# Optimization experiments

Measured on AMD Instinct MI355X. Metric: run time of the kernel, lower is better.

The kernel has to match this reference:

```python
import jax, jax.numpy as jnp
import numpy as np

MARGIN = 0.1
EPS = 1e-8  # torch CosineSimilarity eps


def setup_inputs() -> dict:
    key = jax.random.key(0)
    k1, k2 = jax.random.split(key)
    embeddings = jax.random.normal(k1, (8192, 128), dtype=jnp.float32)
    labels = jax.random.randint(k2, (8192,), 0, 100, dtype=jnp.int64 if jax.config.jax_enable_x64 else jnp.int32)
    return {"embeddings": embeddings, "labels": labels}


def reference(embeddings, labels):
    n = embeddings.shape[0]
    # Normalize rows (torch: x / max(||x||, eps))
    norm = jnp.linalg.norm(embeddings, axis=1, keepdims=True)
    en = embeddings / jnp.maximum(norm, EPS)
    # Full cosine-similarity matrix via one GEMM: [n, n]
    sim = jnp.einsum('id,jd->ij', en, en)
    same = labels[:, None] == labels[None, :]
    pair_loss = jnp.where(same, jax.nn.relu(1.0 - sim), jax.nn.relu(sim - MARGIN))
    # Sum over i < j (strict upper triangle), matching the double loop
    upper = jnp.triu(jnp.ones((n, n), dtype=pair_loss.dtype), k=1)
    loss = jnp.sum(pair_loss * upper) / (n * (n - 1))
    return loss
```

## Files before the change

### kernel.cpp

```cpp
#include <hip/hip_runtime.h>
#include <hip/hip_bf16.h>


typedef __attribute__((ext_vector_type(8))) short short8;
typedef __attribute__((ext_vector_type(4))) float f32x4;

#define DIM 128
#define MARGIN 0.1f
#define CHUNK 4

typedef const void __attribute__((address_space(1)))* gas_ptr;
typedef void __attribute__((address_space(3)))* las_ptr;

static __device__ __forceinline__ void load16_to_lds(const void* g, void* l) {
    __builtin_amdgcn_global_load_lds((gas_ptr)g, (las_ptr)l, 16, 0, 0);
}

static __device__ __forceinline__ unsigned short f2bf(float f) {
    unsigned int u = __builtin_bit_cast(unsigned int, f);
    u += 0x7FFFu + ((u >> 16) & 1u);
    return (unsigned short)(u >> 16);
}

static __device__ __forceinline__ void stage64(const short* __restrict__ en, int row0,
                                               short* buf, int tid) {
    const char* src = (const char*)(en + (size_t)row0 * DIM);
    char* dst = (char*)buf;
    const int r_lo = tid >> 4;
    const int s    = tid & 15;
    #pragma unroll
    for (int p = 0; p < 4; ++p) {
        const int r  = p * 16 + r_lo;
        const int sc = (s ^ (r & 7)) << 4;
        load16_to_lds(src + (size_t)r * 256 + sc, dst + r * 256 + s * 16);
    }
}

static __device__ __forceinline__ short8 read_frag(const short* buf, int row, int slot) {
    const int ps = slot ^ (row & 7);
    return *(const short8*)(buf + row * DIM + ps * 8);
}

__global__ void __launch_bounds__(256) norm_bf16_kernel(const float* __restrict__ e,
                                                        unsigned int* __restrict__ en_packed) {
    const int row  = blockIdx.x * 4 + (threadIdx.x >> 6);
    const int lane = threadIdx.x & 63;
    const float2 v = *reinterpret_cast<const float2*>(e + row * DIM + lane * 2);
    float s = v.x * v.x + v.y * v.y;
    #pragma unroll
    for (int off = 32; off; off >>= 1) s += __shfl_xor(s, off, 64);
    const float scale = 1.0f / fmaxf(sqrtf(s), 1e-8f);
    const unsigned int lo = f2bf(v.x * scale);
    const unsigned int hi = f2bf(v.y * scale);
    en_packed[row * (DIM / 2) + lane] = (hi << 16) | lo;
}

__global__ void __launch_bounds__(256, 3)
tri_loss_kernel(const short* __restrict__ en, const int* __restrict__ labels,
                float* __restrict__ partials, int nt) {
    __shared__ __align__(16) short buf[2][64 * DIM];
    __shared__ float wsum[4];

    int t  = blockIdx.x;
    int bi = 0, cnt = (nt + CHUNK - 1) / CHUNK;
    #pragma unroll 1
    while (t >= cnt) { t -= cnt; ++bi; cnt = (nt - bi + CHUNK - 1) / CHUNK; }
    const int jbase = bi + t * CHUNK;
    const int nsub  = 2 * min(CHUNK, nt - jbase);

    const int tid  = threadIdx.x;
    const int lane = tid & 63;
    const int wid  = tid >> 6;
    const int wr   = wid >> 1, wc = wid & 1;
    const int lm   = lane & 15;
    const int hi   = lane >> 4;

    stage64(en, bi * 128,      &buf[0][0], tid);
    stage64(en, bi * 128 + 64, &buf[1][0], tid);

    const int r0w = bi * 128 + wr * 64;
    int4 li[4];
    #pragma unroll
    for (int m = 0; m < 4; ++m) li[m] = *(const int4*)(labels + r0w + m * 16 + hi * 4);

    __syncthreads();

    short8 a[4][4];
    const short* Abuf = &buf[wr][0];
    #pragma unroll
    for (int m = 0; m < 4; ++m)
        #pragma unroll
        for (int ks = 0; ks < 4; ++ks)
            a[m][ks] = read_frag(Abuf, m * 16 + lm, hi + ks * 4);

    __syncthreads();

    stage64(en, jbase * 128, &buf[0][0], tid);
    __syncthreads();

    float lsum = 0.0f;
    const int rb = hi * 4;

    #pragma unroll 1
    for (int s = 0; s < nsub; ++s) {
        const short* cur = &buf[s & 1][0];
        if (s + 1 < nsub)
            stage64(en, jbase * 128 + (s + 1) * 64, &buf[(s + 1) & 1][0], tid);

        const int c0 = jbase * 128 + s * 64 + wc * 32;
        int labj[2];
        labj[0] = labels[c0 + lm];
        labj[1] = labels[c0 + 16 + lm];

        f32x4 acc[4][2] = {};
        #pragma unroll
        for (int ks = 0; ks < 4; ++ks) {
            short8 b[2];
            b[0] = read_frag(cur, wc * 32 + lm,      hi + ks * 4);
            b[1] = read_frag(cur, wc * 32 + 16 + lm, hi + ks * 4);
            #pragma unroll
            for (int m = 0; m < 4; ++m)
                #pragma unroll
                for (int n = 0; n < 2; ++n)
                    acc[m][n] = __builtin_amdgcn_mfma_f32_16x16x32_bf16(a[m][ks], b[n], acc[m][n], 0, 0, 0);
        }

        const bool diag = (jbase == bi) && (s < 2);
        #pragma unroll
        for (int m = 0; m < 4; ++m) {
            #pragma unroll
            for (int r = 0; r < 4; ++r) {
                const int i   = r0w + m * 16 + rb + r;
                const int l_i = ((const int*)&li[m])[r];
                #pragma unroll
                for (int n = 0; n < 2; ++n) {
                    const int j  = c0 + n * 16 + lm;
                    const float sv = acc[m][n][r];
                    const float t2 = (l_i == labj[n]) ? (1.0f - sv) : (sv - MARGIN);
                    const float v  = fmaxf(t2, 0.0f);
                    if (!diag || i < j) lsum += v;
                }
            }
        }
        __syncthreads();
    }

    #pragma unroll
    for (int off = 32; off; off >>= 1) lsum += __shfl_down(lsum, off, 64);
    if (lane == 0) wsum[wid] = lsum;
    __syncthreads();
    if (tid == 0) partials[blockIdx.x] = wsum[0] + wsum[1] + wsum[2] + wsum[3];
}

__global__ void __launch_bounds__(256) final_reduce_kernel(const float* __restrict__ partials,
                                                           float* __restrict__ out,
                                                           int n, float inv_denom) {
    float s = 0.0f;
    for (int i = threadIdx.x; i < n; i += 256) s += partials[i];
    #pragma unroll
    for (int off = 32; off; off >>= 1) s += __shfl_xor(s, off, 64);
    __shared__ float wsum[4];
    if ((threadIdx.x & 63) == 0) wsum[threadIdx.x >> 6] = s;
    __syncthreads();
    if (threadIdx.x == 0) out[0] = (wsum[0] + wsum[1] + wsum[2] + wsum[3]) * inv_denom;
}

extern "C" void kernel_launch(void* const* d_in, const int* in_sizes, int n_in,
                              void* d_out, int out_size, void* d_ws, size_t ws_size,
                              hipStream_t stream) {
    const float* emb    = (const float*)d_in[0];
    const int*   labels = (const int*)d_in[1];
    float*       out    = (float*)d_out;

    const int n  = in_sizes[1];
    const int nt = n / 128;

    int Tc = 0;
    for (int i = 0; i < nt; ++i) Tc += (nt - i + CHUNK - 1) / CHUNK;

    unsigned int* en_packed = (unsigned int*)d_ws;
    short*        en        = (short*)d_ws;
    float*        partials  = (float*)((char*)d_ws + (size_t)n * DIM * 2);

    norm_bf16_kernel<<<n / 4, 256, 0, stream>>>(emb, en_packed);

    tri_loss_kernel<<<Tc, 256, 0, stream>>>(en, labels, partials, nt);

    const float inv_denom = (float)(1.0 / ((double)n * (double)(n - 1)));
    final_reduce_kernel<<<1, 256, 0, stream>>>(partials, out, Tc, inv_denom);
}
```

Before: 31.00 us.

## Software-pipeline MFMA of next sub-tile with epilogue of current sub-tile

The sub-tile loop now uses two accumulator sets and two label sets, unrolled by two. The MFMAs for sub-tile s+1 are issued before the loss epilogue of sub-tile s, so matrix and vector work can overlap. LDS staging is also pushed one step further ahead, with B-fragment offsets precomputed once. The epilogue is simplified: the diagonal mask is applied only to diagonal tiles, partial sums accumulate in a float4, and the relu on the same-label term is dropped. Holding twice the accumulators raises register pressure, so launch bounds drop from 3 to 2 blocks per CU.

```diff
diff --git a/kernel.cpp b/kernel.cpp
--- a/kernel.cpp
+++ b/kernel.cpp
@@ -55,7 +55,61 @@
     en_packed[row * (DIM / 2) + lane] = (hi << 16) | lo;
 }
 
-__global__ void __launch_bounds__(256, 3)
+
+#define EPI_FAST(ACC, LJ)                                                          \
+    _Pragma("unroll") for (int m = 0; m < 4; ++m)                                  \
+        _Pragma("unroll") for (int n = 0; n < 2; ++n) {                            \
+            const f32x4 sv   = ACC[m][n];                                          \
+            const f32x4 base = sv - MARGIN;                                        \
+            const f32x4 alt  = 1.0f - sv;                                          \
+            _Pragma("unroll") for (int r = 0; r < 4; ++r) {                        \
+                const float bv = fmaxf(base[r], 0.0f);                             \
+                vsum[r] += (liv[m][r] == LJ[n]) ? alt[r] : bv;                     \
+            }                                                                      \
+        }
+
+#define EPI_DIAG(ACC, LJ)                                                          \
+    _Pragma("unroll") for (int m = 0; m < 4; ++m)                                  \
+        _Pragma("unroll") for (int n = 0; n < 2; ++n) {                            \
+            const f32x4 sv   = ACC[m][n];                                          \
+            const f32x4 base = sv - MARGIN;                                        \
+            const f32x4 alt  = 1.0f - sv;                                          \
+            const int jj = c0 + n * 16 + lm;                                       \
+            _Pragma("unroll") for (int r = 0; r < 4; ++r) {                        \
+                const int ii = r0w + m * 16 + rb + r;                              \
+                const float bv = fmaxf(base[r], 0.0f);                             \
+                const float tv = (liv[m][r] == LJ[n]) ? alt[r] : bv;               \
+                vsum[r] += (ii < jj) ? tv : 0.0f;                                  \
+            }                                                                      \
+        }
+
+#define ITER(SX, BSEL, ACC_C, ACC_N, LJ_C, LJ_N) do {                              \
+    const int sx_ = (SX);                                                          \
+    __syncthreads();                                                               \
+    if (sx_ + 2 < nsub) stage64(en, jb128 + (sx_ + 2) * 64, &buf[sx_ & 1][0], tid);\
+    if (sx_ + 1 < nsub) {                                                          \
+        const int c0n = jb128 + (sx_ + 1) * 64 + wc * 32;                          \
+        LJ_N[0] = labels[c0n + lm];                                                \
+        LJ_N[1] = labels[c0n + 16 + lm];                                           \
+        _Pragma("unroll") for (int m = 0; m < 4; ++m)                              \
+            _Pragma("unroll") for (int n = 0; n < 2; ++n)                          \
+                ACC_N[m][n] = (f32x4){0.0f, 0.0f, 0.0f, 0.0f};                     \
+        _Pragma("unroll") for (int ks = 0; ks < 4; ++ks) {                         \
+            const short8 b0 = *(const short8*)(bbase + (BSEL) * 16384 + boff[0][ks]); \
+            const short8 b1 = *(const short8*)(bbase + (BSEL) * 16384 + boff[1][ks]); \
+            _Pragma("unroll") for (int m = 0; m < 4; ++m) {                        \
+                ACC_N[m][0] = __builtin_amdgcn_mfma_f32_16x16x32_bf16(a[m][ks], b0, ACC_N[m][0], 0, 0, 0); \
+                ACC_N[m][1] = __builtin_amdgcn_mfma_f32_16x16x32_bf16(a[m][ks], b1, ACC_N[m][1], 0, 0, 0); \
+            }                                                                      \
+        }                                                                          \
+    }                                                                              \
+    {                                                                              \
+        const int c0 = jb128 + sx_ * 64 + wc * 32; (void)c0;                       \
+        if (hasdiag && sx_ < 2) { EPI_DIAG(ACC_C, LJ_C) } else { EPI_FAST(ACC_C, LJ_C) } \
+    }                                                                              \
+} while (0)
+
+__global__ void __launch_bounds__(256, 2)
 tri_loss_kernel(const short* __restrict__ en, const int* __restrict__ labels,
                 float* __restrict__ partials, int nt) {
     __shared__ __align__(16) short buf[2][64 * DIM];
@@ -66,7 +120,9 @@
     #pragma unroll 1
     while (t >= cnt) { t -= cnt; ++bi; cnt = (nt - bi + CHUNK - 1) / CHUNK; }
     const int jbase = bi + t * CHUNK;
+    const int jb128 = jbase * 128;
     const int nsub  = 2 * min(CHUNK, nt - jbase);
+    const bool hasdiag = (jbase == bi);
 
     const int tid  = threadIdx.x;
     const int lane = tid & 63;
@@ -74,14 +130,18 @@
     const int wr   = wid >> 1, wc = wid & 1;
     const int lm   = lane & 15;
     const int hi   = lane >> 4;
+    const int rb   = hi * 4;
 
     stage64(en, bi * 128,      &buf[0][0], tid);
     stage64(en, bi * 128 + 64, &buf[1][0], tid);
 
     const int r0w = bi * 128 + wr * 64;
-    int4 li[4];
-    #pragma unroll
-    for (int m = 0; m < 4; ++m) li[m] = *(const int4*)(labels + r0w + m * 16 + hi * 4);
+    int liv[4][4];
+    #pragma unroll
+    for (int m = 0; m < 4; ++m) {
+        const int4 v = *(const int4*)(labels + r0w + m * 16 + rb);
+        liv[m][0] = v.x; liv[m][1] = v.y; liv[m][2] = v.z; liv[m][3] = v.w;
+    }
 
     __syncthreads();
 
@@ -93,58 +153,54 @@
         for (int ks = 0; ks < 4; ++ks)
             a[m][ks] = read_frag(Abuf, m * 16 + lm, hi + ks * 4);
 
-    __syncthreads();
-
-    stage64(en, jbase * 128, &buf[0][0], tid);
-    __syncthreads();
-
-    float lsum = 0.0f;
-    const int rb = hi * 4;
-
-    #pragma unroll 1
-    for (int s = 0; s < nsub; ++s) {
-        const short* cur = &buf[s & 1][0];
-        if (s + 1 < nsub)
-            stage64(en, jbase * 128 + (s + 1) * 64, &buf[(s + 1) & 1][0], tid);
-
-        const int c0 = jbase * 128 + s * 64 + wc * 32;
-        int labj[2];
-        labj[0] = labels[c0 + lm];
-        labj[1] = labels[c0 + 16 + lm];
-
-        f32x4 acc[4][2] = {};
+    const char* bbase = (const char*)&buf[0][0];
+    int boff[2][4];
+    #pragma unroll
+    for (int n = 0; n < 2; ++n) {
+        const int row = wc * 32 + n * 16 + lm;
+        #pragma unroll
+        for (int ks = 0; ks < 4; ++ks)
+            boff[n][ks] = row * 256 + (((hi + ks * 4) ^ (row & 7)) << 4);
+    }
+
+    __syncthreads();
+
+    stage64(en, jb128,      &buf[0][0], tid);
+    stage64(en, jb128 + 64, &buf[1][0], tid);
+    __syncthreads();
+
+    f32x4 accA[4][2], accB[4][2];
+    int   ljA[2], ljB[2];
+    f32x4 vsum = (f32x4){0.0f, 0.0f, 0.0f, 0.0f};
+
+    {
+        const int c00 = jb128 + wc * 32;
+        ljA[0] = labels[c00 + lm];
+        ljA[1] = labels[c00 + 16 + lm];
+        #pragma unroll
+        for (int m = 0; m < 4; ++m)
+            #pragma unroll
+            for (int n = 0; n < 2; ++n)
+                accA[m][n] = (f32x4){0.0f, 0.0f, 0.0f, 0.0f};
         #pragma unroll
         for (int ks = 0; ks < 4; ++ks) {
-            short8 b[2];
-            b[0] = read_frag(cur, wc * 32 + lm,      hi + ks * 4);
-            b[1] = read_frag(cur, wc * 32 + 16 + lm, hi + ks * 4);
+            const short8 b0 = *(const short8*)(bbase + boff[0][ks]);
+            const short8 b1 = *(const short8*)(bbase + boff[1][ks]);
             #pragma unroll
-            for (int m = 0; m < 4; ++m)
-                #pragma unroll
-                for (int n = 0; n < 2; ++n)
-                    acc[m][n] = __builtin_amdgcn_mfma_f32_16x16x32_bf16(a[m][ks], b[n], acc[m][n], 0, 0, 0);
-        }
-
-        const bool diag = (jbase == bi) && (s < 2);
-        #pragma unroll
-        for (int m = 0; m < 4; ++m) {
-            #pragma unroll
-            for (int r = 0; r < 4; ++r) {
-                const int i   = r0w + m * 16 + rb + r;
-                const int l_i = ((const int*)&li[m])[r];
-                #pragma unroll
-                for (int n = 0; n < 2; ++n) {
-                    const int j  = c0 + n * 16 + lm;
-                    const float sv = acc[m][n][r];
-                    const float t2 = (l_i == labj[n]) ? (1.0f - sv) : (sv - MARGIN);
-                    const float v  = fmaxf(t2, 0.0f);
-                    if (!diag || i < j) lsum += v;
-                }
+            for (int m = 0; m < 4; ++m) {
+                accA[m][0] = __builtin_amdgcn_mfma_f32_16x16x32_bf16(a[m][ks], b0, accA[m][0], 0, 0, 0);
+                accA[m][1] = __builtin_amdgcn_mfma_f32_16x16x32_bf16(a[m][ks], b1, accA[m][1], 0, 0, 0);
             }
         }
-        __syncthreads();
-    }
-
+    }
+
+    #pragma unroll 1
+    for (int s = 0; s < nsub; s += 2) {
+        ITER(s,     1, accA, accB, ljA, ljB);
+        ITER(s + 1, 0, accB, accA, ljB, ljA);
+    }
+
+    float lsum = vsum[0] + vsum[1] + vsum[2] + vsum[3];
     #pragma unroll
     for (int off = 32; off; off >>= 1) lsum += __shfl_down(lsum, off, 64);
     if (lane == 0) wsum[wid] = lsum;
```

Measured after the change: 32.90 us. +6.1%, slower.

## Split loss into label-agnostic hinge plus per-class correction pass

Applied to the files above, without the earlier changes.

The main GEMM kernel now applies only relu(sim - margin) to every pair, with no label loads or compares. Same-label pairs are fixed up by a separate pass: labels are bucketed with a histogram and compaction kernels, and a per-class kernel computes those pairs' dot products in fp32 and adds relu(1-s) - relu(s-margin). This removes per-element label comparisons from the hot epilogue. The cost is three extra serial launches, a single-block histogram, a label count hardcoded to 100, and per-class dot products that use bf16-rounded values, so they may differ slightly from the MFMA results they cancel.

```diff
diff --git a/kernel.cpp b/kernel.cpp
--- a/kernel.cpp
+++ b/kernel.cpp
@@ -8,6 +8,9 @@
 #define DIM 128
 #define MARGIN 0.1f
 #define CHUNK 4
+#define NLAB 100
+#define CR 48
+#define PD 132
 
 typedef const void __attribute__((address_space(1)))* gas_ptr;
 typedef void __attribute__((address_space(3)))* las_ptr;
@@ -55,9 +58,120 @@
     en_packed[row * (DIM / 2) + lane] = (hi << 16) | lo;
 }
 
+__global__ void __launch_bounds__(256) count_kernel(const int* __restrict__ labels, int n,
+                                                    int* __restrict__ starts) {
+    __shared__ int hist[NLAB];
+    for (int i = threadIdx.x; i < NLAB; i += 256) hist[i] = 0;
+    __syncthreads();
+    for (int i = threadIdx.x; i < n; i += 256) atomicAdd(&hist[labels[i]], 1);
+    __syncthreads();
+    if (threadIdx.x == 0) {
+        int acc = 0;
+        for (int c = 0; c < NLAB; ++c) { starts[c] = acc; acc += hist[c]; }
+        starts[NLAB] = acc;
+    }
+}
+
+__global__ void __launch_bounds__(256) compact_kernel(const int* __restrict__ labels, int n,
+                                                      const int* __restrict__ starts,
+                                                      int* __restrict__ perm) {
+    const int c    = blockIdx.x;
+    const int tid  = threadIdx.x;
+    const int lane = tid & 63;
+    const int wid  = tid >> 6;
+    __shared__ int wcnt[4];
+    __shared__ int running;
+    if (tid == 0) running = 0;
+    __syncthreads();
+    const int base_c = starts[c];
+    for (int base = 0; base < n; base += 256) {
+        const int i = base + tid;
+        const bool pred = (i < n) && (labels[i] == c);
+        const unsigned long long mask = __ballot(pred);
+        const int myrank = __popcll(mask & ((1ULL << lane) - 1ULL));
+        if (lane == 0) wcnt[wid] = __popcll(mask);
+        __syncthreads();
+        int woff = 0;
+        #pragma unroll
+        for (int w = 0; w < 4; ++w) woff += (w < wid) ? wcnt[w] : 0;
+        const int tot = wcnt[0] + wcnt[1] + wcnt[2] + wcnt[3];
+        if (pred) perm[base_c + running + woff + myrank] = i;
+        __syncthreads();
+        if (tid == 0) running += tot;
+        __syncthreads();
+    }
+}
+
+static __device__ __forceinline__ void stage_rows_f32(const short* __restrict__ en,
+                                                      const int* __restrict__ idx, int nu,
+                                                      float* __restrict__ L, int tid) {
+    for (int q = tid; q < nu * 16; q += 256) {
+        const int k = q >> 4, t = q & 15;
+        const int row = idx[k];
+        const short8 v = *(const short8*)(en + (size_t)row * DIM + t * 8);
+        #pragma unroll
+        for (int e = 0; e < 8; ++e) {
+            const unsigned int u = ((unsigned int)(unsigned short)v[e]) << 16;
+            L[k * PD + t * 8 + e] = __builtin_bit_cast(float, u);
+        }
+    }
+}
+
+__global__ void __launch_bounds__(256) corr_kernel(const short* __restrict__ en,
+                                                   const int* __restrict__ starts,
+                                                   const int* __restrict__ perm,
+                                                   float* __restrict__ outc) {
+    __shared__ float LA[CR * PD];
+    __shared__ float LB[CR * PD];
+    __shared__ float wsum[4];
+    const int c   = blockIdx.x;
+    const int s0  = starts[c];
+    const int nc  = starts[c + 1] - s0;
+    const int tid = threadIdx.x;
+
+    float acc = 0.0f;
+    for (int cu = 0; cu < nc; cu += CR) {
+        const int nu = min(CR, nc - cu);
+        __syncthreads();
+        stage_rows_f32(en, perm + s0 + cu, nu, LA, tid);
+        for (int cv = cu; cv < nc; cv += CR) {
+            const int nv = min(CR, nc - cv);
+            __syncthreads();
+            const float* B = LA;
+            if (cv > cu) { stage_rows_f32(en, perm + s0 + cv, nv, LB, tid); B = LB; }
+            __syncthreads();
+            const bool tri = (cv == cu);
+            const float inv_nv = 1.0f / (float)nv;
+            for (int p = tid; p < nu * nv; p += 256) {
+                int u = (int)((float)p * inv_nv);
+                int v = p - u * nv;
+                if (v < 0)        { --u; v += nv; }
+                else if (v >= nv) { ++u; v -= nv; }
+                if (!tri || u < v) {
+                    const float* pa = &LA[u * PD];
+                    const float* pb = &B[v * PD];
+                    float s = 0.0f;
+                    #pragma unroll
+                    for (int d = 0; d < DIM; d += 4) {
+                        const f32x4 va = *(const f32x4*)(pa + d);
+                        const f32x4 vb = *(const f32x4*)(pb + d);
+                        s += va[0] * vb[0] + va[1] * vb[1] + va[2] * vb[2] + va[3] * vb[3];
+                    }
+                    acc += fmaxf(1.0f - s, 0.0f) - fmaxf(s - MARGIN, 0.0f);
+                }
+            }
+        }
+    }
+
+    #pragma unroll
+    for (int off = 32; off; off >>= 1) acc += __shfl_down(acc, off, 64);
+    if ((tid & 63) == 0) wsum[tid >> 6] = acc;
+    __syncthreads();
+    if (tid == 0) outc[c] = wsum[0] + wsum[1] + wsum[2] + wsum[3];
+}
+
 __global__ void __launch_bounds__(256, 3)
-tri_loss_kernel(const short* __restrict__ en, const int* __restrict__ labels,
-                float* __restrict__ partials, int nt) {
+tri_loss_kernel(const short* __restrict__ en, float* __restrict__ partials, int nt) {
     __shared__ __align__(16) short buf[2][64 * DIM];
     __shared__ float wsum[4];
 
@@ -74,15 +188,12 @@
     const int wr   = wid >> 1, wc = wid & 1;
     const int lm   = lane & 15;
     const int hi   = lane >> 4;
+    const int rb   = hi * 4;
 
     stage64(en, bi * 128,      &buf[0][0], tid);
     stage64(en, bi * 128 + 64, &buf[1][0], tid);
 
     const int r0w = bi * 128 + wr * 64;
-    int4 li[4];
-    #pragma unroll
-    for (int m = 0; m < 4; ++m) li[m] = *(const int4*)(labels + r0w + m * 16 + hi * 4);
-
     __syncthreads();
 
     short8 a[4][4];
@@ -98,19 +209,13 @@
     stage64(en, jbase * 128, &buf[0][0], tid);
     __syncthreads();
 
-    float lsum = 0.0f;
-    const int rb = hi * 4;
+    f32x4 vsum = (f32x4){0.0f, 0.0f, 0.0f, 0.0f};
 
     #pragma unroll 1
     for (int s = 0; s < nsub; ++s) {
         const short* cur = &buf[s & 1][0];
         if (s + 1 < nsub)
             stage64(en, jbase * 128 + (s + 1) * 64, &buf[(s + 1) & 1][0], tid);
-
-        const int c0 = jbase * 128 + s * 64 + wc * 32;
-        int labj[2];
-        labj[0] = labels[c0 + lm];
-        labj[1] = labels[c0 + 16 + lm];
 
         f32x4 acc[4][2] = {};
         #pragma unroll
@@ -125,26 +230,36 @@
                     acc[m][n] = __builtin_amdgcn_mfma_f32_16x16x32_bf16(a[m][ks], b[n], acc[m][n], 0, 0, 0);
         }
 
-        const bool diag = (jbase == bi) && (s < 2);
-        #pragma unroll
-        for (int m = 0; m < 4; ++m) {
+        if ((jbase == bi) && (s < 2)) {
+            const int c0 = jbase * 128 + s * 64 + wc * 32;
             #pragma unroll
-            for (int r = 0; r < 4; ++r) {
-                const int i   = r0w + m * 16 + rb + r;
-                const int l_i = ((const int*)&li[m])[r];
+            for (int m = 0; m < 4; ++m)
                 #pragma unroll
                 for (int n = 0; n < 2; ++n) {
-                    const int j  = c0 + n * 16 + lm;
-                    const float sv = acc[m][n][r];
-                    const float t2 = (l_i == labj[n]) ? (1.0f - sv) : (sv - MARGIN);
-                    const float v  = fmaxf(t2, 0.0f);
-                    if (!diag || i < j) lsum += v;
+                    const f32x4 sv = acc[m][n] - MARGIN;
+                    const int jj = c0 + n * 16 + lm;
+                    #pragma unroll
+                    for (int r = 0; r < 4; ++r) {
+                        const int ii = r0w + m * 16 + rb + r;
+                        const float tv = fmaxf(sv[r], 0.0f);
+                        vsum[r] += (ii < jj) ? tv : 0.0f;
+                    }
                 }
-            }
+        } else {
+            #pragma unroll
+            for (int m = 0; m < 4; ++m)
+                #pragma unroll
+                for (int n = 0; n < 2; ++n) {
+                    const f32x4 sv = acc[m][n] - MARGIN;
+                    #pragma unroll
+                    for (int r = 0; r < 4; ++r)
+                        vsum[r] += fmaxf(sv[r], 0.0f);
+                }
         }
         __syncthreads();
     }
 
+    float lsum = vsum[0] + vsum[1] + vsum[2] + vsum[3];
     #pragma unroll
     for (int off = 32; off; off >>= 1) lsum += __shfl_down(lsum, off, 64);
     if (lane == 0) wsum[wid] = lsum;
@@ -178,14 +293,19 @@
     int Tc = 0;
     for (int i = 0; i < nt; ++i) Tc += (nt - i + CHUNK - 1) / CHUNK;
 
-    unsigned int* en_packed = (unsigned int*)d_ws;
-    short*        en        = (short*)d_ws;
-    float*        partials  = (float*)((char*)d_ws + (size_t)n * DIM * 2);
+    char* ws = (char*)d_ws;
+    unsigned int* en_packed = (unsigned int*)ws;
+    short*        en        = (short*)ws;
+    float*        partials  = (float*)(ws + (size_t)n * DIM * 2);
+    int*          starts    = (int*)(partials + Tc + NLAB);
+    int*          perm      = starts + (NLAB + 1);
 
     norm_bf16_kernel<<<n / 4, 256, 0, stream>>>(emb, en_packed);
-
-    tri_loss_kernel<<<Tc, 256, 0, stream>>>(en, labels, partials, nt);
+    count_kernel<<<1, 256, 0, stream>>>(labels, n, starts);
+    compact_kernel<<<NLAB, 256, 0, stream>>>(labels, n, starts, perm);
+    corr_kernel<<<NLAB, 256, 0, stream>>>(en, starts, perm, partials + Tc);
+    tri_loss_kernel<<<Tc, 256, 0, stream>>>(en, partials, nt);
 
     const float inv_denom = (float)(1.0 / ((double)n * (double)(n - 1)));
-    final_reduce_kernel<<<1, 256, 0, stream>>>(partials, out, Tc, inv_denom);
-}
+    final_reduce_kernel<<<1, 256, 0, stream>>>(partials, out, Tc + NLAB, inv_denom);
+}
```

After: 76.56 us. 2.47x slower.

## Sort rows by label so off-diagonal tiles skip label comparisons

Applied to the files above, without the earlier changes.

Adds a prep kernel that, besides normalising rows to bf16, counting-sorts row indices by label into a permutation and a permuted label array. The loss kernel gathers rows through this permutation, so most tile pairs hold disjoint label ranges and take a cheap hinge-only path with no per-element label compare. The double loop over i<j is symmetric, so permuting rows does not change the result. It hardcodes 100 labels and a per-wave bucket capacity of 160, and adds indirect row loads during staging.

```diff
diff --git a/kernel.cpp b/kernel.cpp
--- a/kernel.cpp
+++ b/kernel.cpp
@@ -8,6 +8,8 @@
 #define DIM 128
 #define MARGIN 0.1f
 #define CHUNK 4
+#define NLAB 100
+#define WCAP 160
 
 typedef const void __attribute__((address_space(1)))* gas_ptr;
 typedef void __attribute__((address_space(3)))* las_ptr;
@@ -22,17 +24,19 @@
     return (unsigned short)(u >> 16);
 }
 
-static __device__ __forceinline__ void stage64(const short* __restrict__ en, int row0,
-                                               short* buf, int tid) {
-    const char* src = (const char*)(en + (size_t)row0 * DIM);
+static __device__ __forceinline__ void stage64p(const short* __restrict__ en,
+                                                const int* __restrict__ perm, int row0,
+                                                short* buf, int tid) {
     char* dst = (char*)buf;
     const int r_lo = tid >> 4;
-    const int s    = tid & 15;
+    const int slot = tid & 15;
     #pragma unroll
     for (int p = 0; p < 4; ++p) {
-        const int r  = p * 16 + r_lo;
-        const int sc = (s ^ (r & 7)) << 4;
-        load16_to_lds(src + (size_t)r * 256 + sc, dst + r * 256 + s * 16);
+        const int r    = p * 16 + r_lo;
+        const int srow = perm[row0 + r];
+        const int sc   = (slot ^ (r & 7)) << 4;
+        load16_to_lds((const char*)(en + (size_t)srow * DIM) + sc,
+                      dst + r * 256 + slot * 16);
     }
 }
 
@@ -41,23 +45,78 @@
     return *(const short8*)(buf + row * DIM + ps * 8);
 }
 
-__global__ void __launch_bounds__(256) norm_bf16_kernel(const float* __restrict__ e,
-                                                        unsigned int* __restrict__ en_packed) {
-    const int row  = blockIdx.x * 4 + (threadIdx.x >> 6);
-    const int lane = threadIdx.x & 63;
-    const float2 v = *reinterpret_cast<const float2*>(e + row * DIM + lane * 2);
-    float s = v.x * v.x + v.y * v.y;
-    #pragma unroll
-    for (int off = 32; off; off >>= 1) s += __shfl_xor(s, off, 64);
-    const float scale = 1.0f / fmaxf(sqrtf(s), 1e-8f);
-    const unsigned int lo = f2bf(v.x * scale);
-    const unsigned int hi = f2bf(v.y * scale);
-    en_packed[row * (DIM / 2) + lane] = (hi << 16) | lo;
+__global__ void __launch_bounds__(256) prep_kernel(const float* __restrict__ e,
+                                                   const int* __restrict__ labels, int n,
+                                                   unsigned int* __restrict__ en_packed,
+                                                   int* __restrict__ perm,
+                                                   int* __restrict__ plab) {
+    const int tid  = threadIdx.x;
+    const int lane = tid & 63;
+    const int wid  = tid >> 6;
+    const int nb_norm = n >> 2;
+
+    if ((int)blockIdx.x < nb_norm) {
+        const int row = blockIdx.x * 4 + wid;
+        const float2 v = *reinterpret_cast<const float2*>(e + (size_t)row * DIM + lane * 2);
+        float s = v.x * v.x + v.y * v.y;
+        #pragma unroll
+        for (int off = 32; off; off >>= 1) s += __shfl_xor(s, off, 64);
+        const float scale = 1.0f / fmaxf(sqrtf(s), 1e-8f);
+        const unsigned int lo = f2bf(v.x * scale);
+        const unsigned int hi = f2bf(v.y * scale);
+        en_packed[row * (DIM / 2) + lane] = (hi << 16) | lo;
+        return;
+    }
+
+    const int c = (int)blockIdx.x - nb_norm;
+    __shared__ int hist[NLAB];
+    __shared__ int wlist[4][WCAP];
+    __shared__ int wcnt[4];
+    __shared__ int red[4];
+
+    for (int i = tid; i < NLAB; i += 256) hist[i] = 0;
+    __syncthreads();
+    for (int i = tid; i < n; i += 256) atomicAdd(&hist[labels[i]], 1);
+    __syncthreads();
+
+    int v = (tid < c && tid < NLAB) ? hist[tid] : 0;
+    #pragma unroll
+    for (int off = 32; off; off >>= 1) v += __shfl_xor(v, off, 64);
+    if (lane == 0) red[wid] = v;
+    __syncthreads();
+    const int starts_c = red[0] + red[1] + red[2] + red[3];
+
+    const int nq    = n >> 2;
+    const int wbase = wid * nq;
+    int running = 0;
+    #pragma unroll 1
+    for (int it = 0; it < nq / 64; ++it) {
+        const int i = wbase + it * 64 + lane;
+        const bool pred = (labels[i] == c);
+        const unsigned long long mask = __ballot(pred);
+        const int rank = __popcll(mask & ((1ULL << lane) - 1ULL));
+        if (pred) {
+            const int p = running + rank;
+            if (p < WCAP) wlist[wid][p] = i;
+        }
+        running += __popcll(mask);
+    }
+    if (lane == 0) wcnt[wid] = min(running, WCAP);
+    __syncthreads();
+
+    int off = starts_c;
+    #pragma unroll
+    for (int w = 0; w < 4; ++w) off += (w < wid) ? wcnt[w] : 0;
+    const int cw = wcnt[wid];
+    for (int k = lane; k < cw; k += 64) {
+        perm[off + k] = wlist[wid][k];
+        plab[off + k] = c;
+    }
 }
 
 __global__ void __launch_bounds__(256, 3)
-tri_loss_kernel(const short* __restrict__ en, const int* __restrict__ labels,
-                float* __restrict__ partials, int nt) {
+tri_loss_kernel(const short* __restrict__ en, const int* __restrict__ perm,
+                const int* __restrict__ plab, float* __restrict__ partials, int nt) {
     __shared__ __align__(16) short buf[2][64 * DIM];
     __shared__ float wsum[4];
 
@@ -66,6 +125,7 @@
     #pragma unroll 1
     while (t >= cnt) { t -= cnt; ++bi; cnt = (nt - bi + CHUNK - 1) / CHUNK; }
     const int jbase = bi + t * CHUNK;
+    const int jb128 = jbase * 128;
     const int nsub  = 2 * min(CHUNK, nt - jbase);
 
     const int tid  = threadIdx.x;
@@ -74,14 +134,20 @@
     const int wr   = wid >> 1, wc = wid & 1;
     const int lm   = lane & 15;
     const int hi   = lane >> 4;
-
-    stage64(en, bi * 128,      &buf[0][0], tid);
-    stage64(en, bi * 128 + 64, &buf[1][0], tid);
+    const int rb   = hi * 4;
+
+    stage64p(en, perm, bi * 128,      &buf[0][0], tid);
+    stage64p(en, perm, bi * 128 + 64, &buf[1][0], tid);
 
     const int r0w = bi * 128 + wr * 64;
-    int4 li[4];
-    #pragma unroll
-    for (int m = 0; m < 4; ++m) li[m] = *(const int4*)(labels + r0w + m * 16 + hi * 4);
+    int liv[4][4];
+    #pragma unroll
+    for (int m = 0; m < 4; ++m) {
+        const int4 lv = *(const int4*)(plab + r0w + m * 16 + rb);
+        liv[m][0] = lv.x; liv[m][1] = lv.y; liv[m][2] = lv.z; liv[m][3] = lv.w;
+    }
+    const int rowlo_c = plab[bi * 128];
+    const int rowhi_c = plab[bi * 128 + 127];
 
     __syncthreads();
 
@@ -95,22 +161,16 @@
 
     __syncthreads();
 
-    stage64(en, jbase * 128, &buf[0][0], tid);
-    __syncthreads();
-
-    float lsum = 0.0f;
-    const int rb = hi * 4;
+    stage64p(en, perm, jb128, &buf[0][0], tid);
+    __syncthreads();
+
+    f32x4 vsum = (f32x4){0.0f, 0.0f, 0.0f, 0.0f};
 
     #pragma unroll 1
     for (int s = 0; s < nsub; ++s) {
         const short* cur = &buf[s & 1][0];
         if (s + 1 < nsub)
-            stage64(en, jbase * 128 + (s + 1) * 64, &buf[(s + 1) & 1][0], tid);
-
-        const int c0 = jbase * 128 + s * 64 + wc * 32;
-        int labj[2];
-        labj[0] = labels[c0 + lm];
-        labj[1] = labels[c0 + 16 + lm];
+            stage64p(en, perm, jb128 + (s + 1) * 64, &buf[(s + 1) & 1][0], tid);
 
         f32x4 acc[4][2] = {};
         #pragma unroll
@@ -125,26 +185,59 @@
                     acc[m][n] = __builtin_amdgcn_mfma_f32_16x16x32_bf16(a[m][ks], b[n], acc[m][n], 0, 0, 0);
         }
 
-        const bool diag = (jbase == bi) && (s < 2);
-        #pragma unroll
-        for (int m = 0; m < 4; ++m) {
+        const int  c0     = jb128 + s * 64 + wc * 32;
+        const bool isdiag = (jbase == bi) && (s < 2);
+        const int  ccl    = plab[jb128 + s * 64];
+        const int  cch    = plab[jb128 + s * 64 + 63];
+        const bool labneed = isdiag || (ccl <= rowhi_c && cch >= rowlo_c);
+
+        if (!labneed) {
             #pragma unroll
-            for (int r = 0; r < 4; ++r) {
-                const int i   = r0w + m * 16 + rb + r;
-                const int l_i = ((const int*)&li[m])[r];
+            for (int m = 0; m < 4; ++m)
                 #pragma unroll
                 for (int n = 0; n < 2; ++n) {
-                    const int j  = c0 + n * 16 + lm;
-                    const float sv = acc[m][n][r];
-                    const float t2 = (l_i == labj[n]) ? (1.0f - sv) : (sv - MARGIN);
-                    const float v  = fmaxf(t2, 0.0f);
-                    if (!diag || i < j) lsum += v;
+                    const f32x4 sv = acc[m][n] - MARGIN;
+                    #pragma unroll
+                    for (int r = 0; r < 4; ++r)
+                        vsum[r] += fmaxf(sv[r], 0.0f);
                 }
+        } else {
+            int labj[2];
+            labj[0] = plab[c0 + lm];
+            labj[1] = plab[c0 + 16 + lm];
+            if (isdiag) {
+                #pragma unroll
+                for (int m = 0; m < 4; ++m)
+                    #pragma unroll
+                    for (int n = 0; n < 2; ++n) {
+                        const f32x4 sv = acc[m][n];
+                        const int jj = c0 + n * 16 + lm;
+                        #pragma unroll
+                        for (int r = 0; r < 4; ++r) {
+                            const int ii = r0w + m * 16 + rb + r;
+                            const float bv = fmaxf(sv[r] - MARGIN, 0.0f);
+                            const float tv = (liv[m][r] == labj[n]) ? (1.0f - sv[r]) : bv;
+                            vsum[r] += (ii < jj) ? tv : 0.0f;
+                        }
+                    }
+            } else {
+                #pragma unroll
+                for (int m = 0; m < 4; ++m)
+                    #pragma unroll
+                    for (int n = 0; n < 2; ++n) {
+                        const f32x4 sv = acc[m][n];
+                        #pragma unroll
+                        for (int r = 0; r < 4; ++r) {
+                            const float bv = fmaxf(sv[r] - MARGIN, 0.0f);
+                            vsum[r] += (liv[m][r] == labj[n]) ? (1.0f - sv[r]) : bv;
+                        }
+                    }
             }
         }
         __syncthreads();
     }
 
+    float lsum = vsum[0] + vsum[1] + vsum[2] + vsum[3];
     #pragma unroll
     for (int off = 32; off; off >>= 1) lsum += __shfl_down(lsum, off, 64);
     if (lane == 0) wsum[wid] = lsum;
@@ -178,13 +271,16 @@
     int Tc = 0;
     for (int i = 0; i < nt; ++i) Tc += (nt - i + CHUNK - 1) / CHUNK;
 
-    unsigned int* en_packed = (unsigned int*)d_ws;
-    short*        en        = (short*)d_ws;
-    float*        partials  = (float*)((char*)d_ws + (size_t)n * DIM * 2);
-
-    norm_bf16_kernel<<<n / 4, 256, 0, stream>>>(emb, en_packed);
-
-    tri_loss_kernel<<<Tc, 256, 0, stream>>>(en, labels, partials, nt);
+    char* ws = (char*)d_ws;
+    unsigned int* en_packed = (unsigned int*)ws;
+    short*        en        = (short*)ws;
+    float*        partials  = (float*)(ws + (size_t)n * DIM * 2);
+    int*          perm      = (int*)(ws + (size_t)n * DIM * 2 + 16384);
+    int*          plab      = perm + n;
+
+    prep_kernel<<<n / 4 + NLAB, 256, 0, stream>>>(emb, labels, n, en_packed, perm, plab);
+
+    tri_loss_kernel<<<Tc, 256, 0, stream>>>(en, perm, plab, partials, nt);
 
     const float inv_denom = (float)(1.0 / ((double)n * (double)(n - 1)));
     final_reduce_kernel<<<1, 256, 0, stream>>>(partials, out, Tc, inv_denom);
```

After: 57.84 us. +86.6%, slower.
